# Optimization experiments

Measured on AMD Instinct MI355X. Metric: run time of the kernel, lower is better.

## Reference

```python
import jax, jax.numpy as jnp
import numpy as np

B, S, D_IN, D_OUT, R = 4, 1024, 1024, 1024, 8

def setup_inputs() -> dict:
    key = jax.random.key(0)
    k1, k2, k3, k4, k5 = jax.random.split(key, 5)
    scale = 1.0 / np.sqrt(D_IN)
    return {
        "x": jax.random.normal(k1, (B, S, D_IN), dtype=jnp.float32),
        "A_params": jax.random.normal(k2, (B, S, D_OUT, R), dtype=jnp.float32) * 0.02,
        "B_params": jax.random.normal(k3, (B, S, R, D_IN), dtype=jnp.float32) * 0.02,
        "W": jax.random.normal(k4, (D_OUT, D_IN), dtype=jnp.float32) * scale,
        "b": jax.random.normal(k5, (D_OUT,), dtype=jnp.float32) * scale,
    }

def reference(x, A_params, B_params, W, b):
    # base linear: y = x @ W^T + b  -> [B, S, D_OUT]
    base_out = jnp.einsum('bsi,oi->bso', x, W) + b
    # per-token low-rank update: (x @ B^T) @ A^T
    inter = jnp.einsum('bsi,bsri->bsr', x, B_params)           # [B, S, R]
    adaptation = jnp.einsum('bsr,bsor->bso', inter, A_params)  # [B, S, D_OUT]
    return base_out + adaptation
```

## Files before the change

kernel.cpp:

```cpp
#include <hip/hip_runtime.h>
#include <hip/hip_bf16.h>
#include <stdint.h>

#define TOKENS 4096
#define DIN 1024
#define DOUT 1024
#define RANK 8
#define BM 128
#define BN 64
#define BK 64

typedef __attribute__((ext_vector_type(4))) float f32x4;
typedef __attribute__((ext_vector_type(8))) short short8;

__device__ __forceinline__ unsigned short f2bf(float f) {
    union { float f; unsigned u; } v; v.f = f;
    unsigned r = v.u + 0x7FFFu + ((v.u >> 16) & 1u);
    return (unsigned short)(r >> 16);
}

__global__ __launch_bounds__(256) void k_inter_cvt(const float* __restrict__ x,
                                                   const float* __restrict__ Bp,
                                                   const float* __restrict__ W,
                                                   float* __restrict__ inter,
                                                   ushort* __restrict__ xb,
                                                   ushort* __restrict__ Wb) {
    const int bid = blockIdx.x;
    const int tid = threadIdx.x;

    if (bid >= 1024) {
        const int b2 = bid - 1024;
        const float4* w4 = (const float4*)(W + (size_t)b2 * 4096);
        ushort4* o4 = (ushort4*)(Wb + (size_t)b2 * 4096);
#pragma unroll
        for (int j = 0; j < 4; ++j) {
            float4 v = w4[j * 256 + tid];
            ushort4 u;
            u.x = f2bf(v.x); u.y = f2bf(v.y); u.z = f2bf(v.z); u.w = f2bf(v.w);
            o4[j * 256 + tid] = u;
        }
        return;
    }

    const int lane = tid & 63, wave = tid >> 6;
    const int t = bid * 4 + wave;

    const float4* x4 = (const float4*)(x + (size_t)t * DIN);
    float4 xv[4];
#pragma unroll
    for (int j = 0; j < 4; ++j) xv[j] = x4[j * 64 + lane];

    ushort4* xb4 = (ushort4*)(xb + (size_t)t * DIN);
#pragma unroll
    for (int j = 0; j < 4; ++j) {
        ushort4 u;
        u.x = f2bf(xv[j].x); u.y = f2bf(xv[j].y);
        u.z = f2bf(xv[j].z); u.w = f2bf(xv[j].w);
        xb4[j * 64 + lane] = u;
    }

    const float4* B4 = (const float4*)(Bp + (size_t)t * RANK * DIN);
    float acc[RANK];
#pragma unroll
    for (int r = 0; r < RANK; ++r) {
        float s = 0.f;
#pragma unroll
        for (int j = 0; j < 4; ++j) {
            float4 bv = B4[r * 256 + j * 64 + lane];
            s += bv.x * xv[j].x + bv.y * xv[j].y + bv.z * xv[j].z + bv.w * xv[j].w;
        }
        acc[r] = s;
    }

#pragma unroll
    for (int r = 0; r < RANK; ++r) {
#pragma unroll
        for (int off = 32; off > 0; off >>= 1)
            acc[r] += __shfl_xor(acc[r], off, 64);
    }

    if (lane == 0) {
        float4 lo, hi;
        lo.x = acc[0]; lo.y = acc[1]; lo.z = acc[2]; lo.w = acc[3];
        hi.x = acc[4]; hi.y = acc[5]; hi.z = acc[6]; hi.w = acc[7];
        float4* ip = (float4*)(inter + (size_t)t * RANK);
        ip[0] = lo; ip[1] = hi;
    }
}

__global__ __launch_bounds__(256, 3) void k_gemm_fused(const ushort* __restrict__ Xb,
                                                       const ushort* __restrict__ Wb,
                                                       const float* __restrict__ bias,
                                                       const float* __restrict__ inter,
                                                       const float* __restrict__ Ap,
                                                       float* __restrict__ out) {
    __shared__ ushort As[2][BM * BK];
    __shared__ ushort Bs[2][BN * BK];
    __shared__ float sInter[BM * 8];
    __shared__ float sBias[BN];

    const int tid = threadIdx.x;
    const int lane = tid & 63, wave = tid >> 6;
    const int wm = wave >> 1, wn = wave & 1;

    const int bid = blockIdx.x;
    const int swz = (bid & 7) * 64 + (bid >> 3);
    const int M0 = (swz >> 4) * BM;
    const int N0 = (swz & 15) * BN;

    const int col16 = lane & 15;
    const int kg = lane >> 4;
    const int c8 = col16 & 7;

    ((float4*)sInter)[tid] = ((const float4*)(inter + (size_t)M0 * RANK))[tid];
    if (tid < 16) ((float4*)sBias)[tid] = ((const float4*)(bias + N0))[tid];

    const float* Abase = Ap + ((size_t)(M0 + wm * 64 + kg * 4) * DOUT +
                               (N0 + wn * 32 + col16)) * RANK;

    auto stage = [&](int b, int kt) {
#pragma unroll
        for (int st = 0; st < 4; ++st) {
            int flat = st * 256 + tid;
            int row = flat >> 3, ch = flat & 7;
            int chs = ch ^ (row & 7);
            const ushort* g = Xb + (size_t)(M0 + row) * DIN + kt + chs * 8;
            __builtin_amdgcn_global_load_lds(
                (const __attribute__((address_space(1))) void*)g,
                (__attribute__((address_space(3))) void*)(&As[b][flat * 8]), 16, 0, 0);
        }
#pragma unroll
        for (int st = 0; st < 2; ++st) {
            int flat = st * 256 + tid;
            int row = flat >> 3, ch = flat & 7;
            int chs = ch ^ (row & 7);
            const ushort* g = Wb + (size_t)(N0 + row) * DIN + kt + chs * 8;
            __builtin_amdgcn_global_load_lds(
                (const __attribute__((address_space(1))) void*)g,
                (__attribute__((address_space(3))) void*)(&Bs[b][flat * 8]), 16, 0, 0);
        }
    };

    stage(0, 0);
    asm volatile("s_waitcnt vmcnt(0) lgkmcnt(0)" ::: "memory");
    __builtin_amdgcn_s_barrier();

    f32x4 acc[4][2] = {};

#pragma unroll
    for (int it = 0; it < 16; ++it) {
        const int cur = it & 1;
        if (it < 15) stage(cur ^ 1, (it + 1) * BK);

        const int nf = it >> 3, mf = (it >> 1) & 3, rg0 = (it & 1) * 2;
        const float* Ae0 = Abase + ((size_t)(mf * 16 + rg0) * DOUT + nf * 16) * RANK;
        const float* Ae1 = Ae0 + (size_t)DOUT * RANK;
        float4 a00 = ((const float4*)Ae0)[0];
        float4 a01 = ((const float4*)Ae0)[1];
        float4 a10 = ((const float4*)Ae1)[0];
        float4 a11 = ((const float4*)Ae1)[1];

#pragma unroll
        for (int ks = 0; ks < 2; ++ks) {
            short8 a[4], b[2];
#pragma unroll
            for (int m4 = 0; m4 < 4; ++m4) {
                const int chs = (ks * 4 + kg) ^ c8;
                a[m4] = *(const short8*)(&As[cur][(wm * 64 + m4 * 16 + col16) * BK + chs * 8]);
            }
#pragma unroll
            for (int n2 = 0; n2 < 2; ++n2) {
                const int chs = (ks * 4 + kg) ^ c8;
                b[n2] = *(const short8*)(&Bs[cur][(wn * 32 + n2 * 16 + col16) * BK + chs * 8]);
            }
#pragma unroll
            for (int m4 = 0; m4 < 4; ++m4)
#pragma unroll
                for (int n2 = 0; n2 < 2; ++n2)
                    acc[m4][n2] = __builtin_amdgcn_mfma_f32_16x16x32_bf16(
                        a[m4], b[n2], acc[m4][n2], 0, 0, 0);
        }

        {
            const int mloc0 = wm * 64 + mf * 16 + kg * 4 + rg0;
            const float4* iv0 = (const float4*)(sInter + mloc0 * 8);
            const float4* iv1 = (const float4*)(sInter + (mloc0 + 1) * 8);
            float4 i00 = iv0[0], i01 = iv0[1], i10 = iv1[0], i11 = iv1[1];
            float d0 = a00.x * i00.x + a00.y * i00.y + a00.z * i00.z + a00.w * i00.w +
                       a01.x * i01.x + a01.y * i01.y + a01.z * i01.z + a01.w * i01.w;
            float d1 = a10.x * i10.x + a10.y * i10.y + a10.z * i10.z + a10.w * i10.w +
                       a11.x * i11.x + a11.y * i11.y + a11.z * i11.z + a11.w * i11.w;
            acc[mf][nf][rg0] += d0;
            acc[mf][nf][rg0 + 1] += d1;
        }

        asm volatile("s_waitcnt vmcnt(0)" ::: "memory");
        __builtin_amdgcn_s_barrier();
    }

#pragma unroll
    for (int nf = 0; nf < 2; ++nf) {
        const int oc = wn * 32 + nf * 16 + col16;
        const int o = N0 + oc;
        const float bb = sBias[oc];
#pragma unroll
        for (int mf = 0; mf < 4; ++mf) {
#pragma unroll
            for (int rg = 0; rg < 4; ++rg) {
                const int m = M0 + wm * 64 + mf * 16 + kg * 4 + rg;
                out[(size_t)m * DOUT + o] = acc[mf][nf][rg] + bb;
            }
        }
    }
}

extern "C" void kernel_launch(void* const* d_in, const int* in_sizes, int n_in,
                              void* d_out, int out_size, void* d_ws, size_t ws_size,
                              hipStream_t stream) {
    const float* x    = (const float*)d_in[0];
    const float* Ap   = (const float*)d_in[1];
    const float* Bp   = (const float*)d_in[2];
    const float* W    = (const float*)d_in[3];
    const float* bias = (const float*)d_in[4];
    float* out = (float*)d_out;

    ushort* xb = (ushort*)d_ws;
    ushort* Wb = xb + (size_t)TOKENS * DIN;
    float* inter = (float*)(Wb + (size_t)DOUT * DIN);

    hipLaunchKernelGGL(k_inter_cvt, dim3(1024 + 256), dim3(256), 0, stream,
                       x, Bp, W, inter, xb, Wb);
    hipLaunchKernelGGL(k_gemm_fused, dim3((TOKENS / BM) * (DOUT / BN)), dim3(256), 0, stream,
                       xb, Wb, bias, inter, Ap, out);
}
```

Before: 71.88 us.

## Move low-rank adaptation out of GEMM loop into per-block pre/post phase

The A_params loads and rank-8 dot products, previously spread across the K loop, now run as a separate phase: even blocks do it before the GEMM main loop and odd blocks after it. The intent is to keep the MFMA pipeline free of scattered global loads and to stagger the memory-heavy A_params streaming against the compute-heavy GEMM across co-resident blocks. Bias is now added in that phase from global memory instead of shared memory, and the occupancy hint of 3 blocks per CU is dropped. The A_params loads are no longer hidden under MFMA work, and register pressure may rise.

```diff
diff --git a/kernel.cpp b/kernel.cpp
--- a/kernel.cpp
+++ b/kernel.cpp
@@ -88,16 +88,15 @@
     }
 }
 
-__global__ __launch_bounds__(256, 3) void k_gemm_fused(const ushort* __restrict__ Xb,
-                                                       const ushort* __restrict__ Wb,
-                                                       const float* __restrict__ bias,
-                                                       const float* __restrict__ inter,
-                                                       const float* __restrict__ Ap,
-                                                       float* __restrict__ out) {
+__global__ __launch_bounds__(256) void k_gemm_fused(const ushort* __restrict__ Xb,
+                                                    const ushort* __restrict__ Wb,
+                                                    const float* __restrict__ bias,
+                                                    const float* __restrict__ inter,
+                                                    const float* __restrict__ Ap,
+                                                    float* __restrict__ out) {
     __shared__ ushort As[2][BM * BK];
     __shared__ ushort Bs[2][BN * BK];
     __shared__ float sInter[BM * 8];
-    __shared__ float sBias[BN];
 
     const int tid = threadIdx.x;
     const int lane = tid & 63, wave = tid >> 6;
@@ -107,16 +106,41 @@
     const int swz = (bid & 7) * 64 + (bid >> 3);
     const int M0 = (swz >> 4) * BM;
     const int N0 = (swz & 15) * BN;
+    const int flavor = bid & 1;
 
     const int col16 = lane & 15;
     const int kg = lane >> 4;
     const int c8 = col16 & 7;
 
     ((float4*)sInter)[tid] = ((const float4*)(inter + (size_t)M0 * RANK))[tid];
-    if (tid < 16) ((float4*)sBias)[tid] = ((const float4*)(bias + N0))[tid];
 
     const float* Abase = Ap + ((size_t)(M0 + wm * 64 + kg * 4) * DOUT +
                                (N0 + wn * 32 + col16)) * RANK;
+
+    f32x4 acc[4][2] = {};
+
+    auto adapt_phase = [&]() {
+        const float bb0 = bias[N0 + wn * 32 + col16];
+        const float bb1 = bias[N0 + wn * 32 + 16 + col16];
+#pragma unroll
+        for (int mf = 0; mf < 4; ++mf) {
+#pragma unroll
+            for (int rg = 0; rg < 4; ++rg) {
+                const int mloc = wm * 64 + mf * 16 + kg * 4 + rg;
+                const float4* iv = (const float4*)(sInter + mloc * 8);
+                float4 i0 = iv[0], i1 = iv[1];
+                const float* Ae = Abase + (size_t)(mf * 16 + rg) * DOUT * RANK;
+#pragma unroll
+                for (int nf = 0; nf < 2; ++nf) {
+                    const float4* ap = (const float4*)(Ae + nf * 16 * RANK);
+                    float4 a0 = ap[0], a1 = ap[1];
+                    float d = a0.x * i0.x + a0.y * i0.y + a0.z * i0.z + a0.w * i0.w +
+                              a1.x * i1.x + a1.y * i1.y + a1.z * i1.z + a1.w * i1.w;
+                    acc[mf][nf][rg] += d + (nf ? bb1 : bb0);
+                }
+            }
+        }
+    };
 
     auto stage = [&](int b, int kt) {
 #pragma unroll
@@ -141,25 +165,20 @@
         }
     };
 
+    if (flavor == 0) {
+        __syncthreads();
+        adapt_phase();
+    }
+
     stage(0, 0);
     asm volatile("s_waitcnt vmcnt(0) lgkmcnt(0)" ::: "memory");
     __builtin_amdgcn_s_barrier();
 
-    f32x4 acc[4][2] = {};
-
 #pragma unroll
     for (int it = 0; it < 16; ++it) {
         const int cur = it & 1;
         if (it < 15) stage(cur ^ 1, (it + 1) * BK);
 
-        const int nf = it >> 3, mf = (it >> 1) & 3, rg0 = (it & 1) * 2;
-        const float* Ae0 = Abase + ((size_t)(mf * 16 + rg0) * DOUT + nf * 16) * RANK;
-        const float* Ae1 = Ae0 + (size_t)DOUT * RANK;
-        float4 a00 = ((const float4*)Ae0)[0];
-        float4 a01 = ((const float4*)Ae0)[1];
-        float4 a10 = ((const float4*)Ae1)[0];
-        float4 a11 = ((const float4*)Ae1)[1];
-
 #pragma unroll
         for (int ks = 0; ks < 2; ++ks) {
             short8 a[4], b[2];
@@ -181,34 +200,23 @@
                         a[m4], b[n2], acc[m4][n2], 0, 0, 0);
         }
 
-        {
-            const int mloc0 = wm * 64 + mf * 16 + kg * 4 + rg0;
-            const float4* iv0 = (const float4*)(sInter + mloc0 * 8);
-            const float4* iv1 = (const float4*)(sInter + (mloc0 + 1) * 8);
-            float4 i00 = iv0[0], i01 = iv0[1], i10 = iv1[0], i11 = iv1[1];
-            float d0 = a00.x * i00.x + a00.y * i00.y + a00.z * i00.z + a00.w * i00.w +
-                       a01.x * i01.x + a01.y * i01.y + a01.z * i01.z + a01.w * i01.w;
-            float d1 = a10.x * i10.x + a10.y * i10.y + a10.z * i10.z + a10.w * i10.w +
-                       a11.x * i11.x + a11.y * i11.y + a11.z * i11.z + a11.w * i11.w;
-            acc[mf][nf][rg0] += d0;
-            acc[mf][nf][rg0 + 1] += d1;
-        }
-
         asm volatile("s_waitcnt vmcnt(0)" ::: "memory");
         __builtin_amdgcn_s_barrier();
     }
 
+    if (flavor == 1) {
+        adapt_phase();
+    }
+
 #pragma unroll
     for (int nf = 0; nf < 2; ++nf) {
-        const int oc = wn * 32 + nf * 16 + col16;
-        const int o = N0 + oc;
-        const float bb = sBias[oc];
+        const int o = N0 + wn * 32 + nf * 16 + col16;
 #pragma unroll
         for (int mf = 0; mf < 4; ++mf) {
 #pragma unroll
             for (int rg = 0; rg < 4; ++rg) {
                 const int m = M0 + wm * 64 + mf * 16 + kg * 4 + rg;
-                out[(size_t)m * DOUT + o] = acc[mf][nf][rg] + bb;
+                out[(size_t)m * DOUT + o] = acc[mf][nf][rg];
             }
         }
     }
```

Result: no change. 71.70 us (-0.3%).

## Prefetch A_params one iteration ahead and use partial vmcnt waits

Applied to the files above, without the earlier changes.

Loads the per-token A_params fragments for the next K-iteration into a double-buffered register set, issued together with the next LDS stage. The single trailing full vmcnt wait becomes a partial wait at the top of each iteration, so the current tile's loads can complete while the newest prefetches stay in flight. This is meant to hide global-load latency of the large A_params stream behind the MFMA work. Launch bounds drop from 3 to 2 waves per SIMD to make room for the extra registers, which lowers occupancy and relies on the vmcnt counts matching the issue order.

```diff
diff --git a/kernel.cpp b/kernel.cpp
--- a/kernel.cpp
+++ b/kernel.cpp
@@ -88,7 +88,7 @@
     }
 }
 
-__global__ __launch_bounds__(256, 3) void k_gemm_fused(const ushort* __restrict__ Xb,
+__global__ __launch_bounds__(256, 2) void k_gemm_fused(const ushort* __restrict__ Xb,
                                                        const ushort* __restrict__ Wb,
                                                        const float* __restrict__ bias,
                                                        const float* __restrict__ inter,
@@ -141,24 +141,47 @@
         }
     };
 
+    auto aptr = [&](int e) {
+        const int nf = e >> 3, mf = (e >> 1) & 3, rg0 = (e & 1) * 2;
+        return Abase + ((size_t)(mf * 16 + rg0) * DOUT + nf * 16) * RANK;
+    };
+
+    float4 areg[2][4];
+
+    {
+        const float* Ae0 = aptr(0);
+        areg[0][0] = ((const float4*)Ae0)[0];
+        areg[0][1] = ((const float4*)Ae0)[1];
+        areg[0][2] = ((const float4*)(Ae0 + (size_t)DOUT * RANK))[0];
+        areg[0][3] = ((const float4*)(Ae0 + (size_t)DOUT * RANK))[1];
+    }
+    __builtin_amdgcn_sched_barrier(0);
     stage(0, 0);
-    asm volatile("s_waitcnt vmcnt(0) lgkmcnt(0)" ::: "memory");
-    __builtin_amdgcn_s_barrier();
 
     f32x4 acc[4][2] = {};
 
 #pragma unroll
-    for (int it = 0; it < 16; ++it) {
-        const int cur = it & 1;
-        if (it < 15) stage(cur ^ 1, (it + 1) * BK);
-
-        const int nf = it >> 3, mf = (it >> 1) & 3, rg0 = (it & 1) * 2;
-        const float* Ae0 = Abase + ((size_t)(mf * 16 + rg0) * DOUT + nf * 16) * RANK;
-        const float* Ae1 = Ae0 + (size_t)DOUT * RANK;
-        float4 a00 = ((const float4*)Ae0)[0];
-        float4 a01 = ((const float4*)Ae0)[1];
-        float4 a10 = ((const float4*)Ae1)[0];
-        float4 a11 = ((const float4*)Ae1)[1];
+    for (int t = 0; t < 16; ++t) {
+        const int cur = t & 1;
+
+        if (t < 15) {
+            const float* Ae0 = aptr(t + 1);
+            areg[cur ^ 1][0] = ((const float4*)Ae0)[0];
+            areg[cur ^ 1][1] = ((const float4*)Ae0)[1];
+            areg[cur ^ 1][2] = ((const float4*)(Ae0 + (size_t)DOUT * RANK))[0];
+            areg[cur ^ 1][3] = ((const float4*)(Ae0 + (size_t)DOUT * RANK))[1];
+            __builtin_amdgcn_sched_barrier(0);
+            stage(cur ^ 1, (t + 1) * BK);
+        }
+
+        if (t == 0) {
+            asm volatile("s_waitcnt vmcnt(10) lgkmcnt(0)" ::: "memory");
+        } else if (t < 15) {
+            asm volatile("s_waitcnt vmcnt(10)" ::: "memory");
+        } else {
+            asm volatile("s_waitcnt vmcnt(0)" ::: "memory");
+        }
+        __builtin_amdgcn_s_barrier();
 
 #pragma unroll
         for (int ks = 0; ks < 2; ++ks) {
@@ -182,10 +205,13 @@
         }
 
         {
+            const int nf = t >> 3, mf = (t >> 1) & 3, rg0 = (t & 1) * 2;
             const int mloc0 = wm * 64 + mf * 16 + kg * 4 + rg0;
             const float4* iv0 = (const float4*)(sInter + mloc0 * 8);
             const float4* iv1 = (const float4*)(sInter + (mloc0 + 1) * 8);
             float4 i00 = iv0[0], i01 = iv0[1], i10 = iv1[0], i11 = iv1[1];
+            float4 a00 = areg[cur][0], a01 = areg[cur][1];
+            float4 a10 = areg[cur][2], a11 = areg[cur][3];
             float d0 = a00.x * i00.x + a00.y * i00.y + a00.z * i00.z + a00.w * i00.w +
                        a01.x * i01.x + a01.y * i01.y + a01.z * i01.z + a01.w * i01.w;
             float d1 = a10.x * i10.x + a10.y * i10.y + a10.z * i10.z + a10.w * i10.w +
@@ -194,7 +220,6 @@
             acc[mf][nf][rg0 + 1] += d1;
         }
 
-        asm volatile("s_waitcnt vmcnt(0)" ::: "memory");
         __builtin_amdgcn_s_barrier();
     }
 
```

New measurement: 70.20 us. 1.02x faster.
